# Kernel tuning notes

Hardware: AMD Instinct MI355X
Metric: run time of the kernel (lower is better)

Reference implementation:

```python
import jax, jax.numpy as jnp
import numpy as np

T, H, N = 4096, 2048, 1024  # seq_length, d_model, d_hidden
MAX_PHASE = 6.28


def setup_inputs() -> dict:
    key = jax.random.key(0)
    ks = jax.random.split(key, 9)
    inputs = jax.random.normal(ks[0], (T, H), dtype=jnp.float32)
    # LRU init (exp_param=True, r_min=0, r_max=1): lambda = exp(-exp(nu) + i*exp(theta))
    u1 = jax.random.uniform(ks[1], (N,), dtype=jnp.float32)
    u2 = jax.random.uniform(ks[2], (N,), dtype=jnp.float32)
    nu = jnp.log(-0.5 * jnp.log(u1))            # log-parameterized decay
    theta = jnp.log(MAX_PHASE * u2)             # log-parameterized phase
    # gamma_log = log(sqrt(1 - |lambda|^2)), |lambda| = exp(-exp(nu))
    gamma_log = 0.5 * jnp.log(1.0 - jnp.exp(-2.0 * jnp.exp(nu)) + 1e-8)
    B_re = jax.random.normal(ks[3], (N, H), dtype=jnp.float32) / np.sqrt(2 * H)
    B_im = jax.random.normal(ks[4], (N, H), dtype=jnp.float32) / np.sqrt(2 * H)
    C_re = jax.random.normal(ks[5], (H, N), dtype=jnp.float32) / np.sqrt(N)
    C_im = jax.random.normal(ks[6], (H, N), dtype=jnp.float32) / np.sqrt(N)
    D = jax.random.normal(ks[7], (H,), dtype=jnp.float32)
    return {"inputs": inputs, "nu": nu, "theta": theta, "gamma_log": gamma_log,
            "B_re": B_re, "B_im": B_im, "C_re": C_re, "C_im": C_im, "D": D}


def _binary_operator_diag(q_i, q_j):
    A_i, b_i = q_i
    A_j, b_j = q_j
    return (A_j * A_i, A_j * b_i + b_j)


def reference(inputs, nu, theta, gamma_log, B_re, B_im, C_re, C_im, D):
    # diag_lambda = exp(-exp(nu) + i*exp(theta))   (exp_param=True)
    diag_lambda = jnp.exp(-jnp.exp(nu) + 1j * jnp.exp(theta))      # [N] complex64
    gamma = jnp.exp(gamma_log)                                      # [N]
    B_norm = (B_re + 1j * B_im) * gamma[:, None]                    # [N, H] complex
    # Bu_t = B_norm @ u_t  ->  [T, N]
    Bu = inputs.astype(jnp.complex64) @ B_norm.T
    Lam = jnp.broadcast_to(diag_lambda[None, :], Bu.shape)          # [T, N]
    # parallel scan of diagonal linear recurrence h_t = lambda * h_{t-1} + Bu_t
    _, h = jax.lax.associative_scan(_binary_operator_diag, (Lam, Bu))
    C = C_re + 1j * C_im                                            # [H, N]
    # y_t = Re(C @ h_t) + D * u_t
    y = (h @ C.T).real + D[None, :] * inputs                        # [T, H]
    return y
```

## Files before the change

### kernel.cpp

```cpp
#include <hip/hip_runtime.h>
#include <math.h>

#define T_DIM 4096
#define H_DIM 2048
#define N_DIM 1024
#define N2    2048
#define KK    2048
#define CHUNK 64
#define NCHUNK (T_DIM / CHUNK)
#define NT    (KK / 64)

using u16    = unsigned short;
using u16x4  = __attribute__((ext_vector_type(4))) u16;
using bf16x8 = __attribute__((ext_vector_type(8))) short;
using f32x4  = __attribute__((ext_vector_type(4))) float;

typedef const __attribute__((address_space(1))) u16 glob_u16;
typedef __attribute__((address_space(3))) u16 lds_u16;

__device__ inline void gload16(const u16* g, u16* l) {
    __builtin_amdgcn_global_load_lds((glob_u16*)g, (lds_u16*)l, 16, 0, 0);
}

__device__ inline u16 f2bf(float x) {
    unsigned u = __builtin_bit_cast(unsigned, x);
    u += 0x7fffu + ((u >> 16) & 1u);
    return (u16)(u >> 16);
}
__device__ inline float bf2f(u16 x) {
    return __builtin_bit_cast(float, (unsigned)x << 16);
}

__global__ __launch_bounds__(256) void cvt_u_k(const float* __restrict__ X,
                                               u16* __restrict__ Y) {
    size_t i = ((size_t)blockIdx.x * 256 + threadIdx.x) * 4;
    float4 v = *(const float4*)(X + i);
    u16x4 o = { f2bf(v.x), f2bf(v.y), f2bf(v.z), f2bf(v.w) };
    *(u16x4*)(Y + i) = o;
}

__global__ __launch_bounds__(256) void cvt_b_k(const float* __restrict__ Bre,
                                               const float* __restrict__ Bim,
                                               const float* __restrict__ glog,
                                               u16* __restrict__ Bcat) {
    size_t i = ((size_t)blockIdx.x * 256 + threadIdx.x) * 4;
    int n = (int)(i >> 11);
    size_t h = i & 2047;
    int nn = n & (N_DIM - 1);
    float g = expf(glog[nn]);
    const float* src = (n < N_DIM ? Bre : Bim) + (size_t)nn * H_DIM + h;
    float4 v = *(const float4*)src;
    u16x4 o = { f2bf(v.x * g), f2bf(v.y * g), f2bf(v.z * g), f2bf(v.w * g) };
    *(u16x4*)(Bcat + i) = o;
}

__global__ __launch_bounds__(256) void cvt_c_k(const float* __restrict__ Cre,
                                               const float* __restrict__ Cim,
                                               u16* __restrict__ Ccat) {
    size_t i = ((size_t)blockIdx.x * 256 + threadIdx.x) * 4;
    int hrow = (int)(i >> 11);
    int n = (int)(i & 2047);
    float sgn = 1.f;
    const float* src;
    if (n < N_DIM) src = Cre + (size_t)hrow * N_DIM + n;
    else { src = Cim + (size_t)hrow * N_DIM + (n - N_DIM); sgn = -1.f; }
    float4 v = *(const float4*)src;
    u16x4 o = { f2bf(v.x * sgn), f2bf(v.y * sgn), f2bf(v.z * sgn), f2bf(v.w * sgn) };
    *(u16x4*)(Ccat + i) = o;
}

template <int EPI>
__global__ __launch_bounds__(512, 2) void gemm_pipe(
    const u16* __restrict__ A, const u16* __restrict__ B,
    float* __restrict__ C, const float* __restrict__ D,
    const u16* __restrict__ Ubf)
{
    __shared__ u16 lds[65536];

    const int tid  = threadIdx.x;
    const int wave = tid >> 6, lane = tid & 63;
    const int bm = blockIdx.x >> 4;
    const int bn = blockIdx.x & 15;
    const size_t row0 = (size_t)bm * 256;
    const size_t col0 = (size_t)bn * 128;
    const int wr = wave >> 1, wc = wave & 1;
    const int fr = lane & 15, fq = lane >> 4;

    const int srow = tid >> 3;
    const int skc  = (tid & 7) ^ (srow & 7);
    const u16* aSrc = A + (row0 + srow) * KK + skc * 8;
    const u16* bSrc = B + (col0 + srow) * KK + skc * 8;

    const int aBase = (wr * 64 + fr) * 64;
    const int bBase = (wc * 64 + fr) * 64;
    const int swz0 = ((fq)     ^ (fr & 7)) * 8;
    const int swz1 = ((4 + fq) ^ (fr & 7)) * 8;

    f32x4 acc[4][4] = {};

    auto STAGE_A = [&](int buf, int kt) {
#pragma unroll
        for (int u = 0; u < 4; ++u)
            gload16(aSrc + (size_t)u * 64 * KK + kt * 64,
                    &lds[buf * 16384 + u * 4096 + wave * 512]);
    };
    auto STAGE_B = [&](int buf, int kt) {
#pragma unroll
        for (int u = 0; u < 2; ++u)
            gload16(bSrc + (size_t)u * 64 * KK + kt * 64,
                    &lds[49152 + buf * 8192 + u * 4096 + wave * 512]);
    };
    auto COMPUTE = [&](int abuf, int bbuf) {
        const u16* Ab = &lds[abuf * 16384];
        const u16* Bb = &lds[49152 + bbuf * 8192];
        bf16x8 af[2][4], bfv[2][4];
#pragma unroll
        for (int m = 0; m < 4; ++m) {
            af[0][m] = *(const bf16x8*)&Ab[aBase + m * 1024 + swz0];
            af[1][m] = *(const bf16x8*)&Ab[aBase + m * 1024 + swz1];
        }
#pragma unroll
        for (int n = 0; n < 4; ++n) {
            bfv[0][n] = *(const bf16x8*)&Bb[bBase + n * 1024 + swz0];
            bfv[1][n] = *(const bf16x8*)&Bb[bBase + n * 1024 + swz1];
        }
        __builtin_amdgcn_s_setprio(1);
#pragma unroll
        for (int kk = 0; kk < 2; ++kk)
#pragma unroll
            for (int m = 0; m < 4; ++m)
#pragma unroll
                for (int n = 0; n < 4; ++n)
                    acc[m][n] = __builtin_amdgcn_mfma_f32_16x16x32_bf16(
                        af[kk][m], bfv[kk][n], acc[m][n], 0, 0, 0);
        __builtin_amdgcn_s_setprio(0);
    };

    STAGE_A(0, 0); STAGE_B(0, 0); STAGE_A(1, 1);

    int a_cur = 0;
    for (int t = 0; t < NT - 1; ++t) {
        asm volatile("s_waitcnt vmcnt(4)" ::: "memory");
        __builtin_amdgcn_s_barrier();
        STAGE_B((t + 1) & 1, t + 1);
        if (t + 2 < NT) {
            int a_nxt = a_cur + 2; if (a_nxt >= 3) a_nxt -= 3;
            STAGE_A(a_nxt, t + 2);
        }
        COMPUTE(a_cur, t & 1);
        ++a_cur; if (a_cur == 3) a_cur = 0;
    }
    asm volatile("s_waitcnt vmcnt(0)" ::: "memory");
    __builtin_amdgcn_s_barrier();
    COMPUTE(a_cur, (NT - 1) & 1);

    const int crow = (int)row0 + wr * 64 + fq * 4;
    const int ccol = (int)col0 + wc * 64 + fr;
    float dc[4];
    if constexpr (EPI) {
#pragma unroll
        for (int n = 0; n < 4; ++n) dc[n] = D[ccol + n * 16];
    }
#pragma unroll
    for (int m = 0; m < 4; ++m)
#pragma unroll
        for (int n = 0; n < 4; ++n) {
            int cc = ccol + n * 16;
#pragma unroll
            for (int j = 0; j < 4; ++j) {
                int r = crow + m * 16 + j;
                size_t p = (size_t)r * N2 + cc;
                float v = acc[m][n][j];
                if constexpr (EPI) v += dc[n] * bf2f(Ubf[p]);
                C[p] = v;
            }
        }
}

__global__ __launch_bounds__(256) void scan_local_k(float* __restrict__ Bu,
                                                    const float* __restrict__ nu,
                                                    const float* __restrict__ theta,
                                                    float* __restrict__ car) {
    int idx = blockIdx.x * 256 + threadIdx.x;
    int chan = idx & (N_DIM - 1);
    int chunk = idx >> 10;
    float a = expf(nu[chan]), b = expf(theta[chan]);
    float m = expf(-a), s, c;
    __sincosf(b, &s, &c);
    float lr = m * c, li = m * s;
    float hr = 0.f, hi = 0.f;
    size_t base = (size_t)chunk * CHUNK * N2 + chan;
    for (int i = 0; i < CHUNK; ++i) {
        size_t p = base + (size_t)i * N2;
        float br = Bu[p], bi = Bu[p + N_DIM];
        float nr = fmaf(lr, hr, fmaf(-li, hi, br));
        float ni = fmaf(lr, hi, fmaf(li, hr, bi));
        hr = nr; hi = ni;
        Bu[p] = hr; Bu[p + N_DIM] = hi;
    }
    car[(size_t)chunk * N2 + chan] = hr;
    car[(size_t)chunk * N2 + N_DIM + chan] = hi;
}

__global__ __launch_bounds__(256) void scan_carry_k(float* __restrict__ car,
                                                    const float* __restrict__ nu,
                                                    const float* __restrict__ theta) {
    __shared__ float sR[NCHUNK][65], sI[NCHUNK][65];
    int tid = threadIdx.x;
    int chan0 = blockIdx.x * 64;
    for (int i = tid; i < NCHUNK * 64; i += 256) {
        int ck = i >> 6, c = i & 63;
        sR[ck][c] = car[(size_t)ck * N2 + chan0 + c];
        sI[ck][c] = car[(size_t)ck * N2 + N_DIM + chan0 + c];
    }
    __syncthreads();
    if (tid < 64) {
        int chan = chan0 + tid;
        float a = expf(nu[chan]), b = expf(theta[chan]);
        float m = expf(-(float)CHUNK * a), s, c;
        __sincosf((float)CHUNK * b, &s, &c);
        float lr = m * c, li = m * s;
        float hr = sR[0][tid], hi = sI[0][tid];
        for (int ck = 1; ck < NCHUNK; ++ck) {
            float nr = fmaf(lr, hr, fmaf(-li, hi, sR[ck][tid]));
            float ni = fmaf(lr, hi, fmaf(li, hr, sI[ck][tid]));
            hr = nr; hi = ni;
            sR[ck][tid] = hr; sI[ck][tid] = hi;
        }
    }
    __syncthreads();
    for (int i = tid; i < NCHUNK * 64; i += 256) {
        int ck = i >> 6, c = i & 63;
        car[(size_t)ck * N2 + chan0 + c] = sR[ck][c];
        car[(size_t)ck * N2 + N_DIM + chan0 + c] = sI[ck][c];
    }
}

__global__ __launch_bounds__(256) void fixup_cvt_k(const float* __restrict__ Bu,
                                                   const float* __restrict__ car,
                                                   const float* __restrict__ nu,
                                                   const float* __restrict__ theta,
                                                   u16* __restrict__ Hbf) {
    size_t idx = (size_t)blockIdx.x * 256 + threadIdx.x;
    int chan = (int)(idx & (N_DIM - 1));
    size_t t = idx >> 10;
    int chunk = (int)(t >> 6);
    size_t p = t * N2 + chan;
    float hr = Bu[p], hi = Bu[p + N_DIM];
    if (chunk > 0) {
        float pf = (float)((t & (CHUNK - 1)) + 1);
        float a = expf(nu[chan]), b = expf(theta[chan]);
        float m = expf(-pf * a), s, c;
        __sincosf(pf * b, &s, &c);
        float lr = m * c, li = m * s;
        size_t cp = (size_t)(chunk - 1) * N2 + chan;
        float cr = car[cp], ci = car[cp + N_DIM];
        hr += lr * cr - li * ci;
        hi += lr * ci + li * cr;
    }
    Hbf[p] = f2bf(hr);
    Hbf[p + N_DIM] = f2bf(hi);
}

extern "C" void kernel_launch(void* const* d_in, const int* in_sizes, int n_in,
                              void* d_out, int out_size, void* d_ws, size_t ws_size,
                              hipStream_t stream) {
    const float* U     = (const float*)d_in[0];
    const float* nu    = (const float*)d_in[1];
    const float* theta = (const float*)d_in[2];
    const float* glog  = (const float*)d_in[3];
    const float* Bre   = (const float*)d_in[4];
    const float* Bim   = (const float*)d_in[5];
    const float* Cre   = (const float*)d_in[6];
    const float* Cim   = (const float*)d_in[7];
    const float* Dp    = (const float*)d_in[8];
    float* Y = (float*)d_out;

    u16* Ubf  = (u16*)d_ws;
    u16* Bcat = Ubf + (size_t)T_DIM * H_DIM;
    u16* Ccat = Bcat + (size_t)N2 * H_DIM;
    u16* Hbf  = Ccat + (size_t)H_DIM * N2;
    float* Bu = (float*)(Hbf + (size_t)T_DIM * N2);
    float* car = Bu + (size_t)T_DIM * N2;

    cvt_u_k<<<(T_DIM * H_DIM / 4) / 256, 256, 0, stream>>>(U, Ubf);
    cvt_b_k<<<((size_t)N2 * H_DIM / 4) / 256, 256, 0, stream>>>(Bre, Bim, glog, Bcat);
    cvt_c_k<<<((size_t)H_DIM * N2 / 4) / 256, 256, 0, stream>>>(Cre, Cim, Ccat);

    gemm_pipe<0><<<256, 512, 0, stream>>>(Ubf, Bcat, Bu, nullptr, nullptr);

    scan_local_k<<<(NCHUNK * N_DIM) / 256, 256, 0, stream>>>(Bu, nu, theta, car);
    scan_carry_k<<<N_DIM / 64, 256, 0, stream>>>(car, nu, theta);
    fixup_cvt_k<<<((size_t)T_DIM * N_DIM) / 256, 256, 0, stream>>>(Bu, car, nu, theta, Hbf);

    gemm_pipe<1><<<256, 512, 0, stream>>>(Hbf, Ccat, Y, Dp, Ubf);
}
```

Baseline: 127.2 us.

## Split GEMM k-step into two barrier-synced halves, remap blocks, restructure scan passes

The GEMM main loop is restructured so each 64-wide k tile is processed in two half-steps. Each half loads fragments, issues the next global-to-LDS stage, synchronises with explicit s_barrier/waitcnt, then runs 16 MFMAs, giving finer-grained interleaving of loads and compute. Block indices are remapped so consecutive blocks land on different XCD-like groups, which should improve cache locality. The chunked scan changes from local-scan-write plus fixup to a carry-only pass followed by a rescan that writes bf16 directly. This removes the intermediate fp32 write-back and the per-element exp/sincos fixup, at the cost of reading Bu twice.

```diff
diff --git a/kernel.cpp b/kernel.cpp
--- a/kernel.cpp
+++ b/kernel.cpp
@@ -79,8 +79,9 @@
 
     const int tid  = threadIdx.x;
     const int wave = tid >> 6, lane = tid & 63;
-    const int bm = blockIdx.x >> 4;
-    const int bn = blockIdx.x & 15;
+    const int nbid = (blockIdx.x & 7) * 32 + (blockIdx.x >> 3);
+    const int bm = nbid >> 4;
+    const int bn = nbid & 15;
     const size_t row0 = (size_t)bm * 256;
     const size_t col0 = (size_t)bn * 128;
     const int wr = wave >> 1, wc = wave & 1;
@@ -93,8 +94,7 @@
 
     const int aBase = (wr * 64 + fr) * 64;
     const int bBase = (wc * 64 + fr) * 64;
-    const int swz0 = ((fq)     ^ (fr & 7)) * 8;
-    const int swz1 = ((4 + fq) ^ (fr & 7)) * 8;
+    const int swzk[2] = { ((fq) ^ (fr & 7)) * 8, ((4 + fq) ^ (fr & 7)) * 8 };
 
     f32x4 acc[4][4] = {};
 
@@ -110,49 +110,63 @@
             gload16(bSrc + (size_t)u * 64 * KK + kt * 64,
                     &lds[49152 + buf * 8192 + u * 4096 + wave * 512]);
     };
-    auto COMPUTE = [&](int abuf, int bbuf) {
-        const u16* Ab = &lds[abuf * 16384];
-        const u16* Bb = &lds[49152 + bbuf * 8192];
-        bf16x8 af[2][4], bfv[2][4];
-#pragma unroll
-        for (int m = 0; m < 4; ++m) {
-            af[0][m] = *(const bf16x8*)&Ab[aBase + m * 1024 + swz0];
-            af[1][m] = *(const bf16x8*)&Ab[aBase + m * 1024 + swz1];
-        }
-#pragma unroll
-        for (int n = 0; n < 4; ++n) {
-            bfv[0][n] = *(const bf16x8*)&Bb[bBase + n * 1024 + swz0];
-            bfv[1][n] = *(const bf16x8*)&Bb[bBase + n * 1024 + swz1];
-        }
+
+    STAGE_A(0, 0); STAGE_B(0, 0); STAGE_A(1, 1);
+    asm volatile("s_waitcnt vmcnt(4)\n\ts_barrier" ::: "memory");
+
+    int a_cur = 0;
+#pragma unroll 2
+    for (int t = 0; t < NT; ++t) {
+        const u16* Ab = &lds[a_cur * 16384];
+        const u16* Bb = &lds[49152 + (t & 1) * 8192];
+        bf16x8 af[4], bfv[4];
+
+#pragma unroll
+        for (int m = 0; m < 4; ++m)
+            af[m] = *(const bf16x8*)&Ab[aBase + m * 1024 + swzk[0]];
+#pragma unroll
+        for (int n = 0; n < 4; ++n)
+            bfv[n] = *(const bf16x8*)&Bb[bBase + n * 1024 + swzk[0]];
+        if (t + 1 < NT) STAGE_B((t + 1) & 1, t + 1);
+        asm volatile("s_barrier\n\ts_waitcnt lgkmcnt(0)" ::: "memory");
         __builtin_amdgcn_s_setprio(1);
 #pragma unroll
-        for (int kk = 0; kk < 2; ++kk)
-#pragma unroll
-            for (int m = 0; m < 4; ++m)
-#pragma unroll
-                for (int n = 0; n < 4; ++n)
-                    acc[m][n] = __builtin_amdgcn_mfma_f32_16x16x32_bf16(
-                        af[kk][m], bfv[kk][n], acc[m][n], 0, 0, 0);
+        for (int m = 0; m < 4; ++m)
+#pragma unroll
+            for (int n = 0; n < 4; ++n)
+                acc[m][n] = __builtin_amdgcn_mfma_f32_16x16x32_bf16(
+                    af[m], bfv[n], acc[m][n], 0, 0, 0);
         __builtin_amdgcn_s_setprio(0);
-    };
-
-    STAGE_A(0, 0); STAGE_B(0, 0); STAGE_A(1, 1);
-
-    int a_cur = 0;
-    for (int t = 0; t < NT - 1; ++t) {
-        asm volatile("s_waitcnt vmcnt(4)" ::: "memory");
-        __builtin_amdgcn_s_barrier();
-        STAGE_B((t + 1) & 1, t + 1);
+        asm volatile("s_barrier" ::: "memory");
+
+#pragma unroll
+        for (int m = 0; m < 4; ++m)
+            af[m] = *(const bf16x8*)&Ab[aBase + m * 1024 + swzk[1]];
+#pragma unroll
+        for (int n = 0; n < 4; ++n)
+            bfv[n] = *(const bf16x8*)&Bb[bBase + n * 1024 + swzk[1]];
         if (t + 2 < NT) {
-            int a_nxt = a_cur + 2; if (a_nxt >= 3) a_nxt -= 3;
+            int a_nxt = a_cur - 1; if (a_nxt < 0) a_nxt = 2;
             STAGE_A(a_nxt, t + 2);
         }
-        COMPUTE(a_cur, t & 1);
+        if (t + 2 < NT)
+            asm volatile("s_waitcnt vmcnt(4)\n\ts_barrier\n\ts_waitcnt lgkmcnt(0)" ::: "memory");
+        else if (t + 1 < NT)
+            asm volatile("s_waitcnt vmcnt(0)\n\ts_barrier\n\ts_waitcnt lgkmcnt(0)" ::: "memory");
+        else
+            asm volatile("s_barrier\n\ts_waitcnt lgkmcnt(0)" ::: "memory");
+        __builtin_amdgcn_s_setprio(1);
+#pragma unroll
+        for (int m = 0; m < 4; ++m)
+#pragma unroll
+            for (int n = 0; n < 4; ++n)
+                acc[m][n] = __builtin_amdgcn_mfma_f32_16x16x32_bf16(
+                    af[m], bfv[n], acc[m][n], 0, 0, 0);
+        __builtin_amdgcn_s_setprio(0);
+        asm volatile("s_barrier" ::: "memory");
+
         ++a_cur; if (a_cur == 3) a_cur = 0;
     }
-    asm volatile("s_waitcnt vmcnt(0)" ::: "memory");
-    __builtin_amdgcn_s_barrier();
-    COMPUTE(a_cur, (NT - 1) & 1);
 
     const int crow = (int)row0 + wr * 64 + fq * 4;
     const int ccol = (int)col0 + wc * 64 + fr;
@@ -177,7 +191,7 @@
         }
 }
 
-__global__ __launch_bounds__(256) void scan_local_k(float* __restrict__ Bu,
+__global__ __launch_bounds__(256) void carry_pass_k(const float* __restrict__ Bu,
                                                     const float* __restrict__ nu,
                                                     const float* __restrict__ theta,
                                                     float* __restrict__ car) {
@@ -196,7 +210,6 @@
         float nr = fmaf(lr, hr, fmaf(-li, hi, br));
         float ni = fmaf(lr, hi, fmaf(li, hr, bi));
         hr = nr; hi = ni;
-        Bu[p] = hr; Bu[p + N_DIM] = hi;
     }
     car[(size_t)chunk * N2 + chan] = hr;
     car[(size_t)chunk * N2 + N_DIM + chan] = hi;
@@ -236,30 +249,33 @@
     }
 }
 
-__global__ __launch_bounds__(256) void fixup_cvt_k(const float* __restrict__ Bu,
-                                                   const float* __restrict__ car,
-                                                   const float* __restrict__ nu,
-                                                   const float* __restrict__ theta,
-                                                   u16* __restrict__ Hbf) {
-    size_t idx = (size_t)blockIdx.x * 256 + threadIdx.x;
-    int chan = (int)(idx & (N_DIM - 1));
-    size_t t = idx >> 10;
-    int chunk = (int)(t >> 6);
-    size_t p = t * N2 + chan;
-    float hr = Bu[p], hi = Bu[p + N_DIM];
+__global__ __launch_bounds__(256) void scan_out_k(const float* __restrict__ Bu,
+                                                  const float* __restrict__ car,
+                                                  const float* __restrict__ nu,
+                                                  const float* __restrict__ theta,
+                                                  u16* __restrict__ Hbf) {
+    int idx = blockIdx.x * 256 + threadIdx.x;
+    int chan = idx & (N_DIM - 1);
+    int chunk = idx >> 10;
+    float a = expf(nu[chan]), b = expf(theta[chan]);
+    float m = expf(-a), s, c;
+    __sincosf(b, &s, &c);
+    float lr = m * c, li = m * s;
+    float hr = 0.f, hi = 0.f;
     if (chunk > 0) {
-        float pf = (float)((t & (CHUNK - 1)) + 1);
-        float a = expf(nu[chan]), b = expf(theta[chan]);
-        float m = expf(-pf * a), s, c;
-        __sincosf(pf * b, &s, &c);
-        float lr = m * c, li = m * s;
         size_t cp = (size_t)(chunk - 1) * N2 + chan;
-        float cr = car[cp], ci = car[cp + N_DIM];
-        hr += lr * cr - li * ci;
-        hi += lr * ci + li * cr;
-    }
-    Hbf[p] = f2bf(hr);
-    Hbf[p + N_DIM] = f2bf(hi);
+        hr = car[cp]; hi = car[cp + N_DIM];
+    }
+    size_t base = (size_t)chunk * CHUNK * N2 + chan;
+    for (int i = 0; i < CHUNK; ++i) {
+        size_t p = base + (size_t)i * N2;
+        float br = Bu[p], bi = Bu[p + N_DIM];
+        float nr = fmaf(lr, hr, fmaf(-li, hi, br));
+        float ni = fmaf(lr, hi, fmaf(li, hr, bi));
+        hr = nr; hi = ni;
+        Hbf[p] = f2bf(hr);
+        Hbf[p + N_DIM] = f2bf(hi);
+    }
 }
 
 extern "C" void kernel_launch(void* const* d_in, const int* in_sizes, int n_in,
@@ -289,9 +305,9 @@
 
     gemm_pipe<0><<<256, 512, 0, stream>>>(Ubf, Bcat, Bu, nullptr, nullptr);
 
-    scan_local_k<<<(NCHUNK * N_DIM) / 256, 256, 0, stream>>>(Bu, nu, theta, car);
+    carry_pass_k<<<(NCHUNK * N_DIM) / 256, 256, 0, stream>>>(Bu, nu, theta, car);
     scan_carry_k<<<N_DIM / 64, 256, 0, stream>>>(car, nu, theta);
-    fixup_cvt_k<<<((size_t)T_DIM * N_DIM) / 256, 256, 0, stream>>>(Bu, car, nu, theta, Hbf);
+    scan_out_k<<<(NCHUNK * N_DIM) / 256, 256, 0, stream>>>(Bu, car, nu, theta, Hbf);
 
     gemm_pipe<1><<<256, 512, 0, stream>>>(Hbf, Ccat, Y, Dp, Ubf);
 }
```

New measurement: 121.7 us. 4.3% less time.
